# Performance work log

Measured on AMD Instinct MI355X. Metric: run time of the kernel, lower is better.

## Reference

```python
import jax, jax.numpy as jnp
import numpy as np


def _gcn_conv(h_in, W, b, src, dst, deg_isqrt, n_nodes):
    # PyG GCNConv: out = D^{-1/2} (A + I) D^{-1/2} (h_in @ W) + b
    # src/dst already include self-loops; deg_isqrt precomputed on self-looped graph.
    h = h_in @ W                                   # [N, hid]
    norm = deg_isqrt[src] * deg_isqrt[dst]         # [E+N]
    msg = h[src] * norm[:, None]                   # gather + scale
    agg = jax.ops.segment_sum(msg, dst, num_segments=n_nodes)  # scatter-add
    return agg + b


def setup_inputs() -> dict:
    key = jax.random.key(0)
    ks = jax.random.split(key, 8)
    N, E, P, IN, HID = 100000, 1600000, 400000, 128, 64
    x = jax.random.normal(ks[0], (N, IN), dtype=jnp.float32)
    edge_index = jax.random.randint(ks[1], (2, E), 0, N, dtype=jnp.int64)
    batch = jax.random.randint(ks[2], (N,), 0, 64, dtype=jnp.int64)
    pairs = jax.random.randint(ks[3], (P, 2), 0, N, dtype=jnp.int64)
    s1 = 1.0 / np.sqrt(IN)
    s2 = 1.0 / np.sqrt(HID)
    W1 = jax.random.normal(ks[4], (IN, HID), dtype=jnp.float32) * s1
    b1 = jnp.zeros((HID,), dtype=jnp.float32)
    W2 = jax.random.normal(ks[5], (HID, HID), dtype=jnp.float32) * s2
    b2 = jnp.zeros((HID,), dtype=jnp.float32)
    Wh = jax.random.normal(ks[6], (2 * HID, 1), dtype=jnp.float32) * s2
    bh = jnp.zeros((1,), dtype=jnp.float32)
    return {"x": x, "edge_index": edge_index, "batch": batch, "pairs": pairs,
            "W1": W1, "b1": b1, "W2": W2, "b2": b2, "Wh": Wh, "bh": bh}


def reference(x, edge_index, batch, pairs, W1, b1, W2, b2, Wh, bh):
    n_nodes = x.shape[0]
    loops = jnp.arange(n_nodes, dtype=edge_index.dtype)
    src = jnp.concatenate([edge_index[0], loops])
    dst = jnp.concatenate([edge_index[1], loops])
    # degree on self-looped graph (counted at dst, PyG convention)
    deg = jax.ops.segment_sum(jnp.ones_like(dst, dtype=x.dtype), dst,
                              num_segments=n_nodes)
    deg_isqrt = jnp.where(deg > 0, jax.lax.rsqrt(deg), 0.0)

    h = jax.nn.relu(_gcn_conv(x, W1, b1, src, dst, deg_isqrt, n_nodes))
    h = jax.nn.relu(_gcn_conv(h, W2, b2, src, dst, deg_isqrt, n_nodes))

    emb = jnp.concatenate([h[pairs[:, 0]], h[pairs[:, 1]]], axis=-1)  # [P, 2*hid]
    out = (emb @ Wh + bh)[:, 0]                                        # [P]
    return out
```

## Files before the change

### kernel.cpp

```cpp
#include <hip/hip_runtime.h>

#define THREADS 256
#define BNODES 256
#define PACK_SHIFT 20
#define TILE 2048

__device__ __forceinline__ unsigned short f2bf(float f) {
    unsigned u = __float_as_uint(f);
    unsigned r = (u + 0x7fff + ((u >> 16) & 1)) >> 16;
    return (unsigned short)r;
}
__device__ __forceinline__ float bf2f_lo(unsigned v) { return __uint_as_float(v << 16); }
__device__ __forceinline__ float bf2f_hi(unsigned v) { return __uint_as_float(v & 0xffff0000u); }


__global__ void zero1_kernel(int* __restrict__ a, int n) {
    for (int i = threadIdx.x; i < n; i += 1024) a[i] = 0;
}

__global__ void scan_small_kernel(const int* __restrict__ cnt, int* __restrict__ ptr,
                                  int nb, int total) {
    __shared__ int sh[1024];
    int t = threadIdx.x;
    int v = (t < nb) ? cnt[t] : 0;
    sh[t] = v;
    __syncthreads();
    for (int off = 1; off < 1024; off <<= 1) {
        int add = (t >= off) ? sh[t - off] : 0;
        __syncthreads();
        sh[t] += add;
        __syncthreads();
    }
    if (t < nb) ptr[t] = sh[t] - v;
    if (t == 0) ptr[nb] = total;
}

__global__ __launch_bounds__(512) void block_scatter(const int* __restrict__ src,
                                                     const int* __restrict__ dst,
                                                     int* __restrict__ bucketCur,
                                                     int* __restrict__ ebuf,
                                                     int NB, int CAP, int E) {
    __shared__ int h[1024];
    __shared__ int bb[1024];
    int t = threadIdx.x;
    for (int i = t; i < NB; i += 512) h[i] = 0;
    __syncthreads();
    int e0 = blockIdx.x * TILE;
    int n = min(TILE, E - e0);
    int d[4]; bool has[4];
    #pragma unroll
    for (int k = 0; k < 4; ++k) {
        int j = t + k * 512;
        has[k] = j < n;
        d[k] = has[k] ? dst[e0 + j] : 0;
    }
    #pragma unroll
    for (int k = 0; k < 4; ++k)
        if (has[k]) atomicAdd(&h[d[k] >> 8], 1);
    __syncthreads();
    for (int i = t; i < NB; i += 512) {
        int c = h[i];
        bb[i] = (c > 0) ? (i * CAP + atomicAdd(&bucketCur[i], c)) : 0;
        h[i] = 0;
    }
    __syncthreads();
    int s[4];
    #pragma unroll
    for (int k = 0; k < 4; ++k) {
        int j = t + k * 512;
        s[k] = has[k] ? src[e0 + j] : 0;
    }
    #pragma unroll
    for (int k = 0; k < 4; ++k)
        if (has[k]) {
            int b = d[k] >> 8;
            int pos = bb[b] + atomicAdd(&h[b], 1);
            ebuf[pos] = s[k] | ((d[k] & (BNODES - 1)) << PACK_SHIFT);
        }
}

__global__ __launch_bounds__(256) void bin_fill_kernel(const int* __restrict__ ebuf,
                                                       const int* __restrict__ subptr,
                                                       int* __restrict__ rowptr,
                                                       float* __restrict__ dis,
                                                       int* __restrict__ srcs,
                                                       int NB, int CAP, int N, int E) {
    __shared__ int cntL[BNODES];
    __shared__ int rb[BNODES];
    int b = blockIdx.x;
    int t = threadIdx.x;
    int base = b * BNODES;
    int g0 = subptr[b];
    int cnt = subptr[b + 1] - g0;
    int s0 = b * CAP, s1 = s0 + cnt;
    cntL[t] = 0;
    __syncthreads();
    for (int i = s0 + t; i < s1; i += 256)
        atomicAdd(&cntL[((unsigned)ebuf[i]) >> PACK_SHIFT], 1);
    __syncthreads();
    int myc = cntL[t];
    if (base + t < N) dis[base + t] = rsqrtf((float)myc + 1.0f);
    rb[t] = myc;
    __syncthreads();
    #pragma unroll
    for (int off = 1; off < 256; off <<= 1) {
        int add = (t >= off) ? rb[t - off] : 0;
        __syncthreads();
        rb[t] += add;
        __syncthreads();
    }
    int excl = rb[t] - myc;
    rb[t] = g0 + excl;
    if (base + t < N) rowptr[base + t] = g0 + excl;
    if (b == NB - 1 && t == 0) rowptr[N] = E;
    cntL[t] = 0;
    __syncthreads();
    const int mask = (1 << PACK_SHIFT) - 1;
    for (int i = s0 + t; i < s1; i += 256) {
        int w = ebuf[i];
        int local = ((unsigned)w) >> PACK_SHIFT;
        int pos = rb[local] + atomicAdd(&cntL[local], 1);
        srcs[pos] = w & mask;
    }
}

template<int K, bool SCALE, typename YT>
__global__ __launch_bounds__(256, 4) void gemm_tiled(const float* __restrict__ X,
                                                     const float* __restrict__ W,
                                                     const float* __restrict__ dis,
                                                     YT* __restrict__ Y, int M) {
    __shared__ float Ws[32 * 64];
    __shared__ float Xs[32 * 68];
    const int t = threadIdx.x;

    const int r0 = blockIdx.x * 64;
    const int wave = t >> 6;
    const int lane = t & 63;
    const int tr = lane & 15;
    const int tc = (lane >> 4) + wave * 4;

    float acc[4][4] = {};

    #pragma unroll 1
    for (int kc = 0; kc < K; kc += 32) {
        __syncthreads();
        #pragma unroll
        for (int it = 0; it < 2; ++it) {
            int i = it * 256 + t;
            ((float4*)Ws)[i] = ((const float4*)(W + (size_t)kc * 64))[i];
        }
        #pragma unroll
        for (int it = 0; it < 2; ++it) {
            int i = it * 256 + t;
            int row = i & 63;
            int kq = i >> 6;
            int gr = r0 + row;
            if (gr >= M) gr = M - 1;
            float4 v = *(const float4*)(X + (size_t)gr * K + kc + kq * 4);
            Xs[(kq * 4 + 0) * 68 + row] = v.x;
            Xs[(kq * 4 + 1) * 68 + row] = v.y;
            Xs[(kq * 4 + 2) * 68 + row] = v.z;
            Xs[(kq * 4 + 3) * 68 + row] = v.w;
        }
        __syncthreads();
        #pragma unroll
        for (int kk = 0; kk < 32; ++kk) {
            float4 xv = *(const float4*)(Xs + kk * 68 + tr * 4);
            float4 wv = *(const float4*)(Ws + kk * 64 + tc * 4);
            acc[0][0] = fmaf(xv.x, wv.x, acc[0][0]);
            acc[0][1] = fmaf(xv.x, wv.y, acc[0][1]);
            acc[0][2] = fmaf(xv.x, wv.z, acc[0][2]);
            acc[0][3] = fmaf(xv.x, wv.w, acc[0][3]);
            acc[1][0] = fmaf(xv.y, wv.x, acc[1][0]);
            acc[1][1] = fmaf(xv.y, wv.y, acc[1][1]);
            acc[1][2] = fmaf(xv.y, wv.z, acc[1][2]);
            acc[1][3] = fmaf(xv.y, wv.w, acc[1][3]);
            acc[2][0] = fmaf(xv.z, wv.x, acc[2][0]);
            acc[2][1] = fmaf(xv.z, wv.y, acc[2][1]);
            acc[2][2] = fmaf(xv.z, wv.z, acc[2][2]);
            acc[2][3] = fmaf(xv.z, wv.w, acc[2][3]);
            acc[3][0] = fmaf(xv.w, wv.x, acc[3][0]);
            acc[3][1] = fmaf(xv.w, wv.y, acc[3][1]);
            acc[3][2] = fmaf(xv.w, wv.z, acc[3][2]);
            acc[3][3] = fmaf(xv.w, wv.w, acc[3][3]);
        }
    }

    #pragma unroll
    for (int i = 0; i < 4; ++i) {
        int row = r0 + tr * 4 + i;
        if (row < M) {
            float s = SCALE ? dis[row] : 1.0f;
            if constexpr (sizeof(YT) == 2) {
                ushort4 st;
                st.x = f2bf(acc[i][0] * s);
                st.y = f2bf(acc[i][1] * s);
                st.z = f2bf(acc[i][2] * s);
                st.w = f2bf(acc[i][3] * s);
                *(ushort4*)((unsigned short*)Y + (size_t)row * 64 + tc * 4) = st;
            } else {
                float4 st = make_float4(acc[i][0] * s, acc[i][1] * s,
                                        acc[i][2] * s, acc[i][3] * s);
                *(float4*)((float*)Y + (size_t)row * 64 + tc * 4) = st;
            }
        }
    }
}

template<bool HEAD>
__global__ __launch_bounds__(256) void pull2_kernel(const unsigned* __restrict__ hpre2,
                                                    const int* __restrict__ rowptr,
                                                    const int* __restrict__ srcs,
                                                    const float* __restrict__ dis,
                                                    const float* __restrict__ b,
                                                    const float* __restrict__ Wh,
                                                    float* __restrict__ out,
                                                    float2* __restrict__ s01, int N) {
    int tid = threadIdx.x;
    int lane = tid & 63;
    int half = lane >> 5;
    int sub = lane & 31;
    int eo = sub >> 4;
    int l = sub & 15;
    int node = blockIdx.x * 8 + (tid >> 6) * 2 + half;
    bool valid = node < N;
    int nc = valid ? node : N - 1;
    int i0 = rowptr[nc];
    int end = valid ? rowptr[nc + 1] : i0;

    uint2 sv = *(const uint2*)(hpre2 + (size_t)nc * 32 + 2 * l);
    float a0 = eo ? 0.f : bf2f_lo(sv.x);
    float a1 = eo ? 0.f : bf2f_hi(sv.x);
    float a2 = eo ? 0.f : bf2f_lo(sv.y);
    float a3 = eo ? 0.f : bf2f_hi(sv.y);

    int i = i0 + eo;
    while (__any(i < end)) {
        #pragma unroll
        for (int k = 0; k < 4; ++k) {
            int idx = i + 2 * k;
            bool m = idx < end;
            int s = srcs[m ? idx : 0];
            uint2 v = *(const uint2*)(hpre2 + (size_t)s * 32 + 2 * l);
            a0 += m ? bf2f_lo(v.x) : 0.f;
            a1 += m ? bf2f_hi(v.x) : 0.f;
            a2 += m ? bf2f_lo(v.y) : 0.f;
            a3 += m ? bf2f_hi(v.y) : 0.f;
        }
        i += 8;
    }

    a0 += __shfl_down(a0, 16, 32);
    a1 += __shfl_down(a1, 16, 32);
    a2 += __shfl_down(a2, 16, 32);
    a3 += __shfl_down(a3, 16, 32);

    float d = dis[nc];
    float4 bb = ((const float4*)b)[l];
    float o0 = fmaf(a0, d, bb.x);
    float o1 = fmaf(a1, d, bb.y);
    float o2 = fmaf(a2, d, bb.z);
    float o3 = fmaf(a3, d, bb.w);
    o0 = o0 > 0.f ? o0 : 0.f;
    o1 = o1 > 0.f ? o1 : 0.f;
    o2 = o2 > 0.f ? o2 : 0.f;
    o3 = o3 > 0.f ? o3 : 0.f;

    if (HEAD) {
        float4 w0 = ((const float4*)Wh)[l];
        float4 w1 = ((const float4*)(Wh + 64))[l];
        float p0 = o0 * w0.x + o1 * w0.y + o2 * w0.z + o3 * w0.w;
        float p1 = o0 * w1.x + o1 * w1.y + o2 * w1.z + o3 * w1.w;
        #pragma unroll
        for (int off = 8; off > 0; off >>= 1) {
            p0 += __shfl_down(p0, off, 16);
            p1 += __shfl_down(p1, off, 16);
        }
        if (valid && sub == 0) s01[node] = make_float2(p0, p1);
    } else {
        if (valid && eo == 0)
            *(float4*)(out + (size_t)node * 64 + 4 * l) = make_float4(o0, o1, o2, o3);
    }
}

__global__ void pair_kernel(const float2* __restrict__ s01, const int* __restrict__ pairs,
                            const float* __restrict__ bh, float* __restrict__ out, int P) {
    int p = blockIdx.x * blockDim.x + threadIdx.x;
    if (p < P) {
        int p0 = pairs[2 * (size_t)p];
        int p1 = pairs[2 * (size_t)p + 1];
        out[p] = s01[p0].x + s01[p1].y + bh[0];
    }
}

__global__ void degf_kernel(const int* __restrict__ dst, float* __restrict__ deg, int E) {
    int e = blockIdx.x * blockDim.x + threadIdx.x;
    if (e < E) atomicAdd(&deg[dst[e]], 1.0f);
}
__global__ void rsqrtf_kernel(float* deg, int N) {
    int i = blockIdx.x * blockDim.x + threadIdx.x;
    if (i < N) deg[i] = rsqrtf(deg[i] + 1.0f);
}
__global__ void scatter_kernel(const float* __restrict__ h, const int* __restrict__ src,
                               const int* __restrict__ dst, const float* __restrict__ dis,
                               float* __restrict__ agg, int E, int N) {
    long long idx = (long long)blockIdx.x * blockDim.x + threadIdx.x;
    int e = (int)(idx >> 6);
    int f = (int)(idx & 63);
    if (e >= E + N) return;
    int s, d;
    if (e < E) { s = src[e]; d = dst[e]; } else { s = e - E; d = s; }
    float norm = dis[s] * dis[d];
    atomicAdd(&agg[(size_t)d * 64 + f], h[(size_t)s * 64 + f] * norm);
}
__global__ void bias_relu_kernel(float* __restrict__ buf, const float* __restrict__ b,
                                 long long total) {
    long long i = (long long)blockIdx.x * blockDim.x + threadIdx.x;
    if (i < total) {
        float v = buf[i] + b[(int)(i & 63)];
        buf[i] = v > 0.f ? v : 0.f;
    }
}
__global__ void head_kernel(const float* __restrict__ h, const int* __restrict__ pairs,
                            const float* __restrict__ Wh, const float* __restrict__ bh,
                            float* __restrict__ out, int P) {
    long long idx = (long long)blockIdx.x * blockDim.x + threadIdx.x;
    int p = (int)(idx >> 6);
    int lane = threadIdx.x & 63;
    if (p >= P) return;
    int p0 = pairs[2 * (size_t)p];
    int p1 = pairs[2 * (size_t)p + 1];
    float v = h[(size_t)p0 * 64 + lane] * Wh[lane]
            + h[(size_t)p1 * 64 + lane] * Wh[64 + lane];
    #pragma unroll
    for (int off = 32; off > 0; off >>= 1) v += __shfl_down(v, off);
    if (lane == 0) out[p] = v + bh[0];
}

extern "C" void kernel_launch(void* const* d_in, const int* in_sizes, int n_in,
                              void* d_out, int out_size, void* d_ws, size_t ws_size,
                              hipStream_t stream) {
    const float* x     = (const float*)d_in[0];
    const int*   ei    = (const int*)d_in[1];
    const int*   pairs = (const int*)d_in[3];
    const float* W1    = (const float*)d_in[4];
    const float* b1    = (const float*)d_in[5];
    const float* W2    = (const float*)d_in[6];
    const float* b2    = (const float*)d_in[7];
    const float* Wh    = (const float*)d_in[8];
    const float* bh    = (const float*)d_in[9];

    const int N = in_sizes[0] / 128;
    const int E = in_sizes[1] / 2;
    const int P = in_sizes[3] / 2;
    const int* srcArr = ei;
    const int* dstArr = ei + E;

    const size_t feat_total = (size_t)N * 64;
    const int NB = (N + BNODES - 1) / BNODES;
    const int tileBlocks = (E + TILE - 1) / TILE;
    const int gemm_blocks = (N + 63) / 64;
    const int pull_blocks = (N + 7) / 8;

    auto align512 = [](size_t v) { return (v + 511) & ~(size_t)511; };

    char* ws = (char*)d_ws;
    size_t off = 0;
    float*  dis    = (float*) (ws + off); off += align512((size_t)N * 4);
    int*    rowptr = (int*)   (ws + off); off += align512(((size_t)N + 1) * 4);
    int*    bucketCur = (int*)(ws + off); off += align512((size_t)NB * 4);
    int*    subptr = (int*)   (ws + off); off += align512(((size_t)NB + 1) * 4);
    float2* s01    = (float2*)(ws + off); off += align512((size_t)N * 8);
    int*    srcs   = (int*)   (ws + off); off += align512((size_t)E * 4);
    size_t bufA_bytes = align512((size_t)E * 4 > feat_total * 2 ? (size_t)E * 4
                                                                : feat_total * 2);
    unsigned short* bufA = (unsigned short*)(ws + off); off += bufA_bytes;
    float*  bufB   = (float*) (ws + off); off += align512(feat_total * 4);
    int*    ebuf   = (int*)bufA;

    const int CAP = (int)(bufA_bytes / ((size_t)4 * NB));
    const int avgB = (E + NB - 1) / NB;
    const bool csr_ok = (off <= ws_size) && (NB <= 1024) && (N <= (1 << PACK_SHIFT)) &&
                        (CAP >= avgB + (avgB >> 2) + 1024);

    if (csr_ok) {
        zero1_kernel<<<1, 1024, 0, stream>>>(bucketCur, NB);
        block_scatter<<<tileBlocks, 512, 0, stream>>>(srcArr, dstArr, bucketCur,
                                                      ebuf, NB, CAP, E);
        scan_small_kernel<<<1, 1024, 0, stream>>>(bucketCur, subptr, NB, E);
        bin_fill_kernel<<<NB, 256, 0, stream>>>(ebuf, subptr, rowptr, dis, srcs,
                                                NB, CAP, N, E);

        gemm_tiled<128, true, unsigned short><<<gemm_blocks, THREADS, 0, stream>>>(
            x, W1, dis, bufA, N);
        pull2_kernel<false><<<pull_blocks, THREADS, 0, stream>>>(
            (const unsigned*)bufA, rowptr, srcs, dis, b1, nullptr, bufB, nullptr, N);

        gemm_tiled<64, true, unsigned short><<<gemm_blocks, THREADS, 0, stream>>>(
            bufB, W2, dis, bufA, N);
        pull2_kernel<true><<<pull_blocks, THREADS, 0, stream>>>(
            (const unsigned*)bufA, rowptr, srcs, dis, b2, Wh, nullptr, s01, N);

        pair_kernel<<<(P + THREADS - 1) / THREADS, THREADS, 0, stream>>>(
            s01, pairs, bh, (float*)d_out, P);
    } else {
        size_t o2 = 0;
        float* deg  = (float*)(ws + o2); o2 += align512((size_t)N * 4);
        float* bA   = (float*)(ws + o2); o2 += align512(feat_total * 4);
        float* bB   = (float*)(ws + o2);
        const size_t edge_threads = (size_t)(E + N) * 64;
        const int eblocks = (E + THREADS - 1) / THREADS;

        hipMemsetAsync(deg, 0, (size_t)N * 4, stream);
        degf_kernel<<<eblocks, THREADS, 0, stream>>>(dstArr, deg, E);
        rsqrtf_kernel<<<(N + THREADS - 1) / THREADS, THREADS, 0, stream>>>(deg, N);

        gemm_tiled<128, false, float><<<gemm_blocks, THREADS, 0, stream>>>(x, W1, deg, bA, N);
        hipMemsetAsync(bB, 0, feat_total * 4, stream);
        scatter_kernel<<<(unsigned)((edge_threads + THREADS - 1) / THREADS), THREADS, 0, stream>>>(
            bA, srcArr, dstArr, deg, bB, E, N);
        bias_relu_kernel<<<(unsigned)((feat_total + THREADS - 1) / THREADS), THREADS, 0, stream>>>(
            bB, b1, (long long)feat_total);

        gemm_tiled<64, false, float><<<gemm_blocks, THREADS, 0, stream>>>(bB, W2, deg, bA, N);
        hipMemsetAsync(bB, 0, feat_total * 4, stream);
        scatter_kernel<<<(unsigned)((edge_threads + THREADS - 1) / THREADS), THREADS, 0, stream>>>(
            bA, srcArr, dstArr, deg, bB, E, N);
        bias_relu_kernel<<<(unsigned)((feat_total + THREADS - 1) / THREADS), THREADS, 0, stream>>>(
            bB, b2, (long long)feat_total);

        head_kernel<<<(unsigned)(((size_t)P * 64 + THREADS - 1) / THREADS), THREADS, 0, stream>>>(
            bB, pairs, Wh, bh, (float*)d_out, P);
    }
}
```

Baseline: 177.3 us.

## Drop bucket scan by using padded per-bucket CSR with start/end pairs

Removes the separate bucket-prefix-scan kernel by giving each bucket a fixed-capacity slot, so the CSR becomes padded and indexed by (start,end) int2 pairs per node. The srcs array moves to its own CAP-strided region, bin_fill runs with 512 threads, and block_scatter processes 4096-edge tiles. Pair indices are also loaded as int2. This saves one launch and a serial scan step, at the cost of a larger srcs buffer and a gappy edge layout with less locality.

```diff
diff --git a/kernel.cpp b/kernel.cpp
--- a/kernel.cpp
+++ b/kernel.cpp
@@ -3,7 +3,7 @@
 #define THREADS 256
 #define BNODES 256
 #define PACK_SHIFT 20
-#define TILE 2048
+#define TILE 4096
 
 __device__ __forceinline__ unsigned short f2bf(float f) {
     unsigned u = __float_as_uint(f);
@@ -16,23 +16,6 @@
 
 __global__ void zero1_kernel(int* __restrict__ a, int n) {
     for (int i = threadIdx.x; i < n; i += 1024) a[i] = 0;
-}
-
-__global__ void scan_small_kernel(const int* __restrict__ cnt, int* __restrict__ ptr,
-                                  int nb, int total) {
-    __shared__ int sh[1024];
-    int t = threadIdx.x;
-    int v = (t < nb) ? cnt[t] : 0;
-    sh[t] = v;
-    __syncthreads();
-    for (int off = 1; off < 1024; off <<= 1) {
-        int add = (t >= off) ? sh[t - off] : 0;
-        __syncthreads();
-        sh[t] += add;
-        __syncthreads();
-    }
-    if (t < nb) ptr[t] = sh[t] - v;
-    if (t == 0) ptr[nb] = total;
 }
 
 __global__ __launch_bounds__(512) void block_scatter(const int* __restrict__ src,
@@ -47,15 +30,15 @@
     __syncthreads();
     int e0 = blockIdx.x * TILE;
     int n = min(TILE, E - e0);
-    int d[4]; bool has[4];
-    #pragma unroll
-    for (int k = 0; k < 4; ++k) {
+    int d[8]; bool has[8];
+    #pragma unroll
+    for (int k = 0; k < 8; ++k) {
         int j = t + k * 512;
         has[k] = j < n;
         d[k] = has[k] ? dst[e0 + j] : 0;
     }
     #pragma unroll
-    for (int k = 0; k < 4; ++k)
+    for (int k = 0; k < 8; ++k)
         if (has[k]) atomicAdd(&h[d[k] >> 8], 1);
     __syncthreads();
     for (int i = t; i < NB; i += 512) {
@@ -64,14 +47,14 @@
         h[i] = 0;
     }
     __syncthreads();
-    int s[4];
-    #pragma unroll
-    for (int k = 0; k < 4; ++k) {
+    int s[8];
+    #pragma unroll
+    for (int k = 0; k < 8; ++k) {
         int j = t + k * 512;
         s[k] = has[k] ? src[e0 + j] : 0;
     }
     #pragma unroll
-    for (int k = 0; k < 4; ++k)
+    for (int k = 0; k < 8; ++k)
         if (has[k]) {
             int b = d[k] >> 8;
             int pos = bb[b] + atomicAdd(&h[b], 1);
@@ -79,44 +62,47 @@
         }
 }
 
-__global__ __launch_bounds__(256) void bin_fill_kernel(const int* __restrict__ ebuf,
-                                                       const int* __restrict__ subptr,
-                                                       int* __restrict__ rowptr,
+__global__ __launch_bounds__(512) void bin_fill_kernel(const int* __restrict__ ebuf,
+                                                       const int* __restrict__ bucketCnt,
+                                                       int2* __restrict__ rowptr2,
                                                        float* __restrict__ dis,
                                                        int* __restrict__ srcs,
-                                                       int NB, int CAP, int N, int E) {
+                                                       int CAP, int N) {
     __shared__ int cntL[BNODES];
     __shared__ int rb[BNODES];
     int b = blockIdx.x;
     int t = threadIdx.x;
     int base = b * BNODES;
-    int g0 = subptr[b];
-    int cnt = subptr[b + 1] - g0;
+    int cnt = bucketCnt[b];
     int s0 = b * CAP, s1 = s0 + cnt;
-    cntL[t] = 0;
-    __syncthreads();
-    for (int i = s0 + t; i < s1; i += 256)
+    if (t < BNODES) cntL[t] = 0;
+    __syncthreads();
+    for (int i = s0 + t; i < s1; i += 512)
         atomicAdd(&cntL[((unsigned)ebuf[i]) >> PACK_SHIFT], 1);
     __syncthreads();
-    int myc = cntL[t];
-    if (base + t < N) dis[base + t] = rsqrtf((float)myc + 1.0f);
-    rb[t] = myc;
-    __syncthreads();
-    #pragma unroll
-    for (int off = 1; off < 256; off <<= 1) {
-        int add = (t >= off) ? rb[t - off] : 0;
+    int myc = 0;
+    if (t < BNODES) {
+        myc = cntL[t];
+        if (base + t < N) dis[base + t] = rsqrtf((float)myc + 1.0f);
+        rb[t] = myc;
+    }
+    __syncthreads();
+    #pragma unroll
+    for (int off = 1; off < BNODES; off <<= 1) {
+        int add = (t < BNODES && t >= off) ? rb[t - off] : 0;
         __syncthreads();
-        rb[t] += add;
+        if (t < BNODES) rb[t] += add;
         __syncthreads();
     }
-    int excl = rb[t] - myc;
-    rb[t] = g0 + excl;
-    if (base + t < N) rowptr[base + t] = g0 + excl;
-    if (b == NB - 1 && t == 0) rowptr[N] = E;
-    cntL[t] = 0;
+    if (t < BNODES) {
+        int start = s0 + rb[t] - myc;
+        if (base + t < N) rowptr2[base + t] = make_int2(start, start + myc);
+        rb[t] = start;
+        cntL[t] = 0;
+    }
     __syncthreads();
     const int mask = (1 << PACK_SHIFT) - 1;
-    for (int i = s0 + t; i < s1; i += 256) {
+    for (int i = s0 + t; i < s1; i += 512) {
         int w = ebuf[i];
         int local = ((unsigned)w) >> PACK_SHIFT;
         int pos = rb[local] + atomicAdd(&cntL[local], 1);
@@ -209,7 +195,7 @@
 
 template<bool HEAD>
 __global__ __launch_bounds__(256) void pull2_kernel(const unsigned* __restrict__ hpre2,
-                                                    const int* __restrict__ rowptr,
+                                                    const int2* __restrict__ rowptr2,
                                                     const int* __restrict__ srcs,
                                                     const float* __restrict__ dis,
                                                     const float* __restrict__ b,
@@ -225,8 +211,9 @@
     int node = blockIdx.x * 8 + (tid >> 6) * 2 + half;
     bool valid = node < N;
     int nc = valid ? node : N - 1;
-    int i0 = rowptr[nc];
-    int end = valid ? rowptr[nc + 1] : i0;
+    int2 se = rowptr2[nc];
+    int i0 = se.x;
+    int end = valid ? se.y : i0;
 
     uint2 sv = *(const uint2*)(hpre2 + (size_t)nc * 32 + 2 * l);
     float a0 = eo ? 0.f : bf2f_lo(sv.x);
@@ -240,7 +227,7 @@
         for (int k = 0; k < 4; ++k) {
             int idx = i + 2 * k;
             bool m = idx < end;
-            int s = srcs[m ? idx : 0];
+            int s = srcs[m ? idx : i0];
             uint2 v = *(const uint2*)(hpre2 + (size_t)s * 32 + 2 * l);
             a0 += m ? bf2f_lo(v.x) : 0.f;
             a1 += m ? bf2f_hi(v.x) : 0.f;
@@ -283,13 +270,12 @@
     }
 }
 
-__global__ void pair_kernel(const float2* __restrict__ s01, const int* __restrict__ pairs,
+__global__ void pair_kernel(const float2* __restrict__ s01, const int2* __restrict__ pairs,
                             const float* __restrict__ bh, float* __restrict__ out, int P) {
     int p = blockIdx.x * blockDim.x + threadIdx.x;
     if (p < P) {
-        int p0 = pairs[2 * (size_t)p];
-        int p1 = pairs[2 * (size_t)p + 1];
-        out[p] = s01[p0].x + s01[p1].y + bh[0];
+        int2 pr = pairs[p];
+        out[p] = s01[pr.x].x + s01[pr.y].y + bh[0];
     }
 }
 
@@ -366,17 +352,16 @@
 
     char* ws = (char*)d_ws;
     size_t off = 0;
-    float*  dis    = (float*) (ws + off); off += align512((size_t)N * 4);
-    int*    rowptr = (int*)   (ws + off); off += align512(((size_t)N + 1) * 4);
-    int*    bucketCur = (int*)(ws + off); off += align512((size_t)NB * 4);
-    int*    subptr = (int*)   (ws + off); off += align512(((size_t)NB + 1) * 4);
-    float2* s01    = (float2*)(ws + off); off += align512((size_t)N * 8);
-    int*    srcs   = (int*)   (ws + off); off += align512((size_t)E * 4);
+    float*  dis     = (float*) (ws + off); off += align512((size_t)N * 4);
+    int2*   rowptr2 = (int2*)  (ws + off); off += align512((size_t)N * 8);
+    int*    bucketCur = (int*) (ws + off); off += align512((size_t)NB * 4);
+    float2* s01     = (float2*)(ws + off); off += align512((size_t)N * 8);
     size_t bufA_bytes = align512((size_t)E * 4 > feat_total * 2 ? (size_t)E * 4
                                                                 : feat_total * 2);
     unsigned short* bufA = (unsigned short*)(ws + off); off += bufA_bytes;
-    float*  bufB   = (float*) (ws + off); off += align512(feat_total * 4);
-    int*    ebuf   = (int*)bufA;
+    int*    srcs    = (int*)   (ws + off); off += bufA_bytes;
+    float*  bufB    = (float*) (ws + off); off += align512(feat_total * 4);
+    int*    ebuf    = (int*)bufA;
 
     const int CAP = (int)(bufA_bytes / ((size_t)4 * NB));
     const int avgB = (E + NB - 1) / NB;
@@ -387,22 +372,21 @@
         zero1_kernel<<<1, 1024, 0, stream>>>(bucketCur, NB);
         block_scatter<<<tileBlocks, 512, 0, stream>>>(srcArr, dstArr, bucketCur,
                                                       ebuf, NB, CAP, E);
-        scan_small_kernel<<<1, 1024, 0, stream>>>(bucketCur, subptr, NB, E);
-        bin_fill_kernel<<<NB, 256, 0, stream>>>(ebuf, subptr, rowptr, dis, srcs,
-                                                NB, CAP, N, E);
+        bin_fill_kernel<<<NB, 512, 0, stream>>>(ebuf, bucketCur, rowptr2, dis, srcs,
+                                                CAP, N);
 
         gemm_tiled<128, true, unsigned short><<<gemm_blocks, THREADS, 0, stream>>>(
             x, W1, dis, bufA, N);
         pull2_kernel<false><<<pull_blocks, THREADS, 0, stream>>>(
-            (const unsigned*)bufA, rowptr, srcs, dis, b1, nullptr, bufB, nullptr, N);
+            (const unsigned*)bufA, rowptr2, srcs, dis, b1, nullptr, bufB, nullptr, N);
 
         gemm_tiled<64, true, unsigned short><<<gemm_blocks, THREADS, 0, stream>>>(
             bufB, W2, dis, bufA, N);
         pull2_kernel<true><<<pull_blocks, THREADS, 0, stream>>>(
-            (const unsigned*)bufA, rowptr, srcs, dis, b2, Wh, nullptr, s01, N);
+            (const unsigned*)bufA, rowptr2, srcs, dis, b2, Wh, nullptr, s01, N);
 
         pair_kernel<<<(P + THREADS - 1) / THREADS, THREADS, 0, stream>>>(
-            s01, pairs, bh, (float*)d_out, P);
+            s01, (const int2*)pairs, bh, (float*)d_out, P);
     } else {
         size_t o2 = 0;
         float* deg  = (float*)(ws + o2); o2 += align512((size_t)N * 4);
```

After: 161.9 us. 1.1x faster.
